# Performance work log

Measured on AMD Instinct MI355X. Metric: run time of the kernel, lower is better.

The kernel has to match this reference:

```python
import jax, jax.numpy as jnp
import numpy as np

N = 100000
E = 3200000
IN_C = 128
HID = 128


def setup_inputs() -> dict:
    key = jax.random.key(0)
    k1, k2, k3, k4, k5 = jax.random.split(key, 5)
    x = jax.random.normal(k1, (N, IN_C), dtype=jnp.float32)
    edge_index = jax.random.randint(k2, (2, E), 0, N, dtype=jnp.int64)
    edge_weight = jax.random.uniform(k3, (E,), dtype=jnp.float32)
    # GCNConv linear weight [out, in] (applied as x @ W.T), glorot-ish scale
    W = jax.random.normal(k4, (HID, IN_C), dtype=jnp.float32) / np.sqrt(IN_C)
    bias = jnp.zeros((HID,), dtype=jnp.float32)
    # PReLU per-channel alpha, torch default init 0.25
    alpha = jnp.full((HID,), 0.25, dtype=jnp.float32)
    return {"x": x, "edge_index": edge_index, "edge_weight": edge_weight,
            "W": W, "bias": bias, "alpha": alpha}


def reference(x, edge_index, edge_weight, W, bias, alpha):
    n = x.shape[0]
    # gcn_norm with self-loops (fill value 1.0)
    loop_idx = jnp.arange(n, dtype=edge_index.dtype)
    row = jnp.concatenate([edge_index[0], loop_idx])  # source
    col = jnp.concatenate([edge_index[1], loop_idx])  # target
    ew = jnp.concatenate([edge_weight, jnp.ones((n,), dtype=edge_weight.dtype)])
    deg = jax.ops.segment_sum(ew, col, num_segments=n)  # in-degree by weight
    dinv = jnp.where(deg > 0, jax.lax.rsqrt(deg), 0.0)
    norm = dinv[row] * ew * dinv[col]  # [E+N]
    # linear transform first (GCNConv order), then gather-scatter aggregation
    h = x @ W.T  # [N, HID]
    msgs = norm[:, None] * h[row]  # [E+N, HID]
    out = jax.ops.segment_sum(msgs, col, num_segments=n) + bias  # [N, HID]
    # PReLU with per-channel alpha
    return jnp.where(out > 0, out, alpha * out)
```

## Files before the change

### kernel.cpp

```cpp
#include <hip/hip_runtime.h>


#define NBLK    512
#define MAXBKT  1600
#define QSCALE  32767.0f
#define Q9      511.0f
#define SBS     16

typedef float vfloat2 __attribute__((ext_vector_type(2)));

__device__ __forceinline__ unsigned bf16pack2(float a, float b) {
    unsigned ua = __float_as_uint(a);
    ua = (ua + 0x7fffu + ((ua >> 16) & 1u)) >> 16;
    unsigned ub = __float_as_uint(b);
    ub = (ub + 0x7fffu + ((ub >> 16) & 1u)) >> 16;
    return ua | (ub << 16);
}

__device__ __forceinline__ float2 bf16unpack2(unsigned u) {
    return make_float2(__uint_as_float(u << 16),
                       __uint_as_float(u & 0xffff0000u));
}

__global__ __launch_bounds__(256) void p1_hist(const int* __restrict__ col,
                                               unsigned* __restrict__ hist,
                                               int e, int nbkt, int epb) {
    __shared__ unsigned lh[MAXBKT];
    int b = blockIdx.x;
    for (int k = threadIdx.x; k < nbkt; k += 256) lh[k] = 0;
    __syncthreads();
    int s = b * epb, en = s + epb; if (en > e) en = e;
    for (int i = s + threadIdx.x; i < en; i += 256)
        atomicAdd(&lh[col[i] >> 6], 1u);
    __syncthreads();
    for (int k = threadIdx.x; k < nbkt; k += 256)
        hist[(size_t)k * NBLK + b] = lh[k];
}

__global__ __launch_bounds__(1024) void scan_partial2(
    const unsigned* __restrict__ a, unsigned* __restrict__ part, int m) {
    __shared__ unsigned red[1024];
    int t = threadIdx.x, i = blockIdx.x * 1024 + t;
    red[t] = (i < m) ? a[i] : 0;
    __syncthreads();
    #pragma unroll
    for (int d = 512; d > 0; d >>= 1) {
        if (t < d) red[t] += red[t + d];
        __syncthreads();
    }
    if (t == 0) part[blockIdx.x] = red[0];
}

__global__ __launch_bounds__(1024) void scan_base2(
    unsigned* __restrict__ part, int nb, int* __restrict__ offs, int n, int e) {
    __shared__ unsigned s[1024];
    int t = threadIdx.x;
    unsigned v = (t < nb) ? part[t] : 0;
    s[t] = v;
    __syncthreads();
    for (int d = 1; d < 1024; d <<= 1) {
        unsigned add = (t >= d) ? s[t - d] : 0;
        __syncthreads();
        s[t] += add;
        __syncthreads();
    }
    if (t < nb) part[t] = s[t] - v;
    if (t == 0) offs[n] = e;
}

__global__ __launch_bounds__(1024) void scan_write2(
    unsigned* __restrict__ a, const unsigned* __restrict__ part, int m) {
    __shared__ unsigned s[1024];
    int t = threadIdx.x, i = blockIdx.x * 1024 + t;
    unsigned v = (i < m) ? a[i] : 0;
    s[t] = v;
    __syncthreads();
    for (int d = 1; d < 1024; d <<= 1) {
        unsigned add = (t >= d) ? s[t - d] : 0;
        __syncthreads();
        s[t] += add;
        __syncthreads();
    }
    if (i < m) a[i] = part[blockIdx.x] + s[t] - v;
}

__global__ __launch_bounds__(256) void fused_p2_gemm(
    const int* __restrict__ col, const int* __restrict__ row,
    const float* __restrict__ ew, const unsigned* __restrict__ base,
    unsigned* __restrict__ pay, int e, int nbkt, int epb,
    const float* __restrict__ x, const float* __restrict__ W,
    unsigned* __restrict__ h, int n) {
    __shared__ float smem[128 * 128];
    int bid = blockIdx.x;
    int t = threadIdx.x;

    if (bid < NBLK) {
        unsigned* lbase = (unsigned*)smem;
        unsigned* lcur  = (unsigned*)smem + MAXBKT;
        int b = bid;
        for (int k = t; k < nbkt; k += 256) {
            lbase[k] = base[(size_t)k * NBLK + b];
            lcur[k] = 0;
        }
        __syncthreads();
        int s = b * epb, en = s + epb; if (en > e) en = e;
        for (int i = s + t; i < en; i += 256) {
            int c = col[i];
            int bk = c >> 6;
            unsigned q = (unsigned)(ew[i] * Q9 + 0.5f);
            unsigned rk = atomicAdd(&lcur[bk], 1u);
            pay[(size_t)lbase[bk] + rk] =
                ((unsigned)(c & 63) << 26) | ((unsigned)row[i] << 9) | q;
        }
        return;
    }

    float (*Wt)[128] = (float (*)[128])smem;
    const float4* W4 = (const float4*)W;
    #pragma unroll
    for (int it = 0; it < 16; ++it) {
        int i = t + it * 256;
        float4 v = W4[i];
        int o  = i >> 5;
        int kb = (i & 31) << 2;
        Wt[kb + 0][o ^ (((kb + 0) & 7) << 2)] = v.x;
        Wt[kb + 1][o ^ (((kb + 1) & 7) << 2)] = v.y;
        Wt[kb + 2][o ^ (((kb + 2) & 7) << 2)] = v.z;
        Wt[kb + 3][o ^ (((kb + 3) & 7) << 2)] = v.w;
    }
    __syncthreads();

    int tc = t & 31;
    int rs = t >> 5;
    int r0 = (bid - NBLK) * 64 + rs * 8;
    if (r0 >= n) return;
    const float4* x4 = (const float4*)x;

    float acc[8][4];
    #pragma unroll
    for (int ri = 0; ri < 8; ++ri)
        #pragma unroll
        for (int j = 0; j < 4; ++j) acc[ri][j] = 0.0f;

    int rcnt = n - r0; if (rcnt > 8) rcnt = 8;

    if (rcnt == 8) {
        for (int kq = 0; kq < 32; ++kq) {
            int kb = kq << 2;
            float4 wv0 = *(const float4*)&Wt[kb + 0][(4 * tc) ^ (((kb + 0) & 7) << 2)];
            float4 wv1 = *(const float4*)&Wt[kb + 1][(4 * tc) ^ (((kb + 1) & 7) << 2)];
            float4 wv2 = *(const float4*)&Wt[kb + 2][(4 * tc) ^ (((kb + 2) & 7) << 2)];
            float4 wv3 = *(const float4*)&Wt[kb + 3][(4 * tc) ^ (((kb + 3) & 7) << 2)];
            #pragma unroll
            for (int ri = 0; ri < 8; ++ri) {
                float4 xv = x4[(size_t)(r0 + ri) * 32 + kq];
                acc[ri][0] += xv.x * wv0.x + xv.y * wv1.x + xv.z * wv2.x + xv.w * wv3.x;
                acc[ri][1] += xv.x * wv0.y + xv.y * wv1.y + xv.z * wv2.y + xv.w * wv3.y;
                acc[ri][2] += xv.x * wv0.z + xv.y * wv1.z + xv.z * wv2.z + xv.w * wv3.z;
                acc[ri][3] += xv.x * wv0.w + xv.y * wv1.w + xv.z * wv2.w + xv.w * wv3.w;
            }
        }
        uint2* h2 = (uint2*)h;
        #pragma unroll
        for (int ri = 0; ri < 8; ++ri)
            h2[(size_t)(r0 + ri) * 32 + tc] =
                make_uint2(bf16pack2(acc[ri][0], acc[ri][1]),
                           bf16pack2(acc[ri][2], acc[ri][3]));
    } else {
        for (int kq = 0; kq < 32; ++kq) {
            int kb = kq << 2;
            float4 wv0 = *(const float4*)&Wt[kb + 0][(4 * tc) ^ (((kb + 0) & 7) << 2)];
            float4 wv1 = *(const float4*)&Wt[kb + 1][(4 * tc) ^ (((kb + 1) & 7) << 2)];
            float4 wv2 = *(const float4*)&Wt[kb + 2][(4 * tc) ^ (((kb + 2) & 7) << 2)];
            float4 wv3 = *(const float4*)&Wt[kb + 3][(4 * tc) ^ (((kb + 3) & 7) << 2)];
            for (int ri = 0; ri < rcnt; ++ri) {
                float4 xv = x4[(size_t)(r0 + ri) * 32 + kq];
                acc[ri][0] += xv.x * wv0.x + xv.y * wv1.x + xv.z * wv2.x + xv.w * wv3.x;
                acc[ri][1] += xv.x * wv0.y + xv.y * wv1.y + xv.z * wv2.y + xv.w * wv3.y;
                acc[ri][2] += xv.x * wv0.z + xv.y * wv1.z + xv.z * wv2.z + xv.w * wv3.z;
                acc[ri][3] += xv.x * wv0.w + xv.y * wv1.w + xv.z * wv2.w + xv.w * wv3.w;
            }
        }
        uint2* h2 = (uint2*)h;
        for (int ri = 0; ri < rcnt; ++ri)
            h2[(size_t)(r0 + ri) * 32 + tc] =
                make_uint2(bf16pack2(acc[ri][0], acc[ri][1]),
                           bf16pack2(acc[ri][2], acc[ri][3]));
    }
}

__global__ __launch_bounds__(256) void p3_build(
    const unsigned* __restrict__ pay,
    const unsigned* __restrict__ histBase,
    unsigned* __restrict__ csr, int* __restrict__ offs,
    float* __restrict__ dinv, int n, int nbkt, int e) {
    __shared__ unsigned cnt[64][SBS], lofs[64][SBS], cur[64][SBS];
    __shared__ unsigned wsum[64], tbase[64], ttot[64];
    int bk = blockIdx.x;
    int zs = (int)histBase[(size_t)bk * NBLK];
    int ze = (bk + 1 < nbkt) ? (int)histBase[(size_t)(bk + 1) * NBLK] : e;
    int t = threadIdx.x;
    for (int k = t; k < 64 * SBS; k += 256) {
        (&cnt[0][0])[k] = 0;
        (&cur[0][0])[k] = 0;
    }
    if (t < 64) wsum[t] = 0;
    __syncthreads();
    for (int p = zs + t; p < ze; p += 256) {
        unsigned v = pay[p];
        int l = (int)(v >> 26);
        int sb = (int)(((v >> 9) & 0x1ffffu) >> 13);
        atomicAdd(&cnt[l][sb], 1u);
        atomicAdd(&wsum[l], v & 0x1ffu);
    }
    __syncthreads();
    if (t < 64) {
        unsigned s = 0;
        #pragma unroll
        for (int j = 0; j < SBS; ++j) s += cnt[t][j];
        ttot[t] = s;
    }
    __syncthreads();
    if (t == 0) {
        unsigned run = 0;
        for (int l = 0; l < 64; ++l) { tbase[l] = run; run += ttot[l]; }
    }
    __syncthreads();
    if (t < 64) {
        unsigned run = tbase[t];
        #pragma unroll
        for (int j = 0; j < SBS; ++j) { lofs[t][j] = run; run += cnt[t][j]; }
    }
    __syncthreads();
    for (int p = zs + t; p < ze; p += 256) {
        unsigned v = pay[p];
        int l = (int)(v >> 26);
        unsigned lo = v & 0x03ffffffu;
        int sb = (int)((lo >> 9) >> 13);
        unsigned rk = atomicAdd(&cur[l][sb], 1u);
        csr[zs + lofs[l][sb] + rk] = lo;
    }
    if (t < 64) {
        int node = bk * 64 + t;
        if (node < n) {
            offs[node] = zs + (int)tbase[t];
            float dg = 1.0f + (float)wsum[t] * (1.0f / Q9);
            dinv[node] = rsqrtf(dg);
        }
    }
}

__global__ __launch_bounds__(256) void csr2_fill(const unsigned* __restrict__ csr,
                                                 const float* __restrict__ dinv,
                                                 unsigned* __restrict__ csr2, int e) {
    int i = blockIdx.x * 256 + threadIdx.x;
    if (i < e) {
        unsigned v = csr[i];
        unsigned src = v >> 9;
        float a = dinv[src] * ((float)(v & 0x1ffu) * (1.0f / Q9));
        csr2[i] = (src << 15) | (unsigned)(a * QSCALE + 0.5f);
    }
}

__global__ __launch_bounds__(256) void aggregate_kernel(
    const unsigned* __restrict__ h, const unsigned* __restrict__ csr2,
    const int* __restrict__ offs, const float* __restrict__ dinv,
    const float* __restrict__ bias, const float* __restrict__ alpha,
    float* __restrict__ out, int n, int swzq) {
    int bid = blockIdx.x;
    int sb  = swzq ? ((bid & 7) * swzq + (bid >> 3)) : bid;
    int w = sb * 4 + (threadIdx.x >> 6);
    if (w >= n) return;
    int lane = threadIdx.x & 63;

    int beg = __builtin_amdgcn_readfirstlane(offs[w]);
    int end = __builtin_amdgcn_readfirstlane(offs[w + 1]);
    float ax = 0.0f, ay = 0.0f;

    int i = beg;
    int end4 = beg + ((end - beg) & ~3);
    for (; i < end4; i += 4) {
        unsigned v0 = __builtin_nontemporal_load(&csr2[i]);
        unsigned v1 = __builtin_nontemporal_load(&csr2[i + 1]);
        unsigned v2 = __builtin_nontemporal_load(&csr2[i + 2]);
        unsigned v3 = __builtin_nontemporal_load(&csr2[i + 3]);
        unsigned u0 = h[(size_t)(v0 >> 15) * 64 + lane];
        unsigned u1 = h[(size_t)(v1 >> 15) * 64 + lane];
        unsigned u2 = h[(size_t)(v2 >> 15) * 64 + lane];
        unsigned u3 = h[(size_t)(v3 >> 15) * 64 + lane];
        float a0 = (float)(v0 & 0x7fffu) * (1.0f / QSCALE);
        float a1 = (float)(v1 & 0x7fffu) * (1.0f / QSCALE);
        float a2 = (float)(v2 & 0x7fffu) * (1.0f / QSCALE);
        float a3 = (float)(v3 & 0x7fffu) * (1.0f / QSCALE);
        float2 h0 = bf16unpack2(u0), h1 = bf16unpack2(u1);
        float2 h2 = bf16unpack2(u2), h3 = bf16unpack2(u3);
        ax += a0 * h0.x; ay += a0 * h0.y;
        ax += a1 * h1.x; ay += a1 * h1.y;
        ax += a2 * h2.x; ay += a2 * h2.y;
        ax += a3 * h3.x; ay += a3 * h3.y;
    }
    for (; i < end; ++i) {
        unsigned v = __builtin_nontemporal_load(&csr2[i]);
        unsigned u = h[(size_t)(v >> 15) * 64 + lane];
        float a = (float)(v & 0x7fffu) * (1.0f / QSCALE);
        float2 hv = bf16unpack2(u);
        ax += a * hv.x; ay += a * hv.y;
    }

    float dc = dinv[w];
    float2 hc = bf16unpack2(h[(size_t)w * 64 + lane]);
    ax += dc * hc.x; ay += dc * hc.y;

    float2 bv = ((const float2*)bias)[lane];
    float2 av = ((const float2*)alpha)[lane];
    float ox = ax * dc + bv.x;
    float oy = ay * dc + bv.y;
    ox = ox > 0.0f ? ox : av.x * ox;
    oy = oy > 0.0f ? oy : av.y * oy;
    vfloat2 ov; ov.x = ox; ov.y = oy;
    __builtin_nontemporal_store(ov,
        (vfloat2*)&((float2*)out)[(size_t)w * 64 + lane]);
}

extern "C" void kernel_launch(void* const* d_in, const int* in_sizes, int n_in,
                              void* d_out, int out_size, void* d_ws, size_t ws_size,
                              hipStream_t stream) {
    const float* x     = (const float*)d_in[0];
    const int*   ei    = (const int*)d_in[1];
    const float* ew    = (const float*)d_in[2];
    const float* W     = (const float*)d_in[3];
    const float* bias  = (const float*)d_in[4];
    const float* alpha = (const float*)d_in[5];
    float* out = (float*)d_out;

    const int n = in_sizes[0] / 128;
    const int e = in_sizes[1] / 2;
    const int* row = ei;
    const int* col = ei + e;

    const int nbkt = (n + 63) >> 6;
    const int m    = nbkt * NBLK;
    const int epb  = (e + NBLK - 1) / NBLK;
    const int nb2  = (m + 1023) / 1024;

    char* ws = (char*)d_ws;
    size_t off = 0;
    auto alloc = [&](size_t bytes) -> char* {
        char* p = ws + off;
        off = (off + bytes + 255) & ~(size_t)255;
        return p;
    };
    unsigned* hist = (unsigned*)alloc((size_t)m * 4);
    unsigned* part = (unsigned*)alloc((size_t)1024 * 4);
    int*      offs = (int*)     alloc((size_t)(n + 1) * 4);
    float*    dinv = (float*)   alloc((size_t)n * 4);
    unsigned* pay  = (unsigned*)alloc((size_t)e * 4);
    unsigned* csr  = (unsigned*)alloc((size_t)e * 4);
    unsigned* csr2 = (unsigned*)alloc((size_t)e * 4);
    unsigned* h    = (unsigned*)alloc((size_t)n * 128 * 2);
    (void)ws_size; (void)n_in; (void)out_size;

    int gg = (n + 63) / 64;

    p1_hist<<<NBLK, 256, 0, stream>>>(col, hist, e, nbkt, epb);
    scan_partial2<<<nb2, 1024, 0, stream>>>(hist, part, m);
    scan_base2<<<1, 1024, 0, stream>>>(part, nb2, offs, n, e);
    scan_write2<<<nb2, 1024, 0, stream>>>(hist, part, m);
    fused_p2_gemm<<<NBLK + gg, 256, 0, stream>>>(col, row, ew, hist, pay,
                                                 e, nbkt, epb, x, W, h, n);
    p3_build<<<nbkt, 256, 0, stream>>>(pay, hist, csr, offs, dinv, n, nbkt, e);
    csr2_fill<<<(e + 255) / 256, 256, 0, stream>>>(csr, dinv, csr2, e);

    int ga = (n + 3) / 4;
    int swzq = (ga % 8 == 0) ? ga / 8 : 0;
    aggregate_kernel<<<ga, 256, 0, stream>>>(h, csr2, offs, dinv,
                                             bias, alpha, out, n, swzq);
}
```

Measured before the change: 288.1 us.

## Split fused scatter/GEMM kernel, shrink partition blocks, add nontemporal edge loads

Splits the fused scatter+GEMM kernel into a standalone 1024-thread scatter kernel and a GEMM kernel launched after the CSR build. It also cuts the partition block count from 512 to 128 with 1024 threads each, and marks streaming edge reads as nontemporal. Fewer, larger blocks shrink the histogram and scan arrays, and the scatter kernel no longer carries the GEMM's 64KB shared-memory footprint. In exchange, the GEMM no longer overlaps with the scatter, and each block's local atomics see more contention.

Result: slower. 332.4 us (+15.4%).

```diff
diff --git a/kernel.cpp b/kernel.cpp
--- a/kernel.cpp
+++ b/kernel.cpp
@@ -1,7 +1,7 @@
 #include <hip/hip_runtime.h>
 
 
-#define NBLK    512
+#define NBLK    128
 #define MAXBKT  1600
 #define QSCALE  32767.0f
 #define Q9      511.0f
@@ -22,18 +22,19 @@
                        __uint_as_float(u & 0xffff0000u));
 }
 
-__global__ __launch_bounds__(256) void p1_hist(const int* __restrict__ col,
-                                               unsigned* __restrict__ hist,
-                                               int e, int nbkt, int epb) {
+__global__ __launch_bounds__(1024) void p1_hist(const int* __restrict__ col,
+                                                unsigned* __restrict__ hist,
+                                                int e, int nbkt, int epb) {
     __shared__ unsigned lh[MAXBKT];
     int b = blockIdx.x;
-    for (int k = threadIdx.x; k < nbkt; k += 256) lh[k] = 0;
+    int t = threadIdx.x;
+    for (int k = t; k < nbkt; k += 1024) lh[k] = 0;
     __syncthreads();
     int s = b * epb, en = s + epb; if (en > e) en = e;
-    for (int i = s + threadIdx.x; i < en; i += 256)
-        atomicAdd(&lh[col[i] >> 6], 1u);
-    __syncthreads();
-    for (int k = threadIdx.x; k < nbkt; k += 256)
+    for (int i = s + t; i < en; i += 1024)
+        atomicAdd(&lh[__builtin_nontemporal_load(&col[i]) >> 6], 1u);
+    __syncthreads();
+    for (int k = t; k < nbkt; k += 1024)
         hist[(size_t)k * NBLK + b] = lh[k];
 }
 
@@ -84,38 +85,110 @@
     if (i < m) a[i] = part[blockIdx.x] + s[t] - v;
 }
 
-__global__ __launch_bounds__(256) void fused_p2_gemm(
+__global__ __launch_bounds__(1024) void p2_scatter(
     const int* __restrict__ col, const int* __restrict__ row,
     const float* __restrict__ ew, const unsigned* __restrict__ base,
-    unsigned* __restrict__ pay, int e, int nbkt, int epb,
-    const float* __restrict__ x, const float* __restrict__ W,
-    unsigned* __restrict__ h, int n) {
-    __shared__ float smem[128 * 128];
-    int bid = blockIdx.x;
-    int t = threadIdx.x;
-
-    if (bid < NBLK) {
-        unsigned* lbase = (unsigned*)smem;
-        unsigned* lcur  = (unsigned*)smem + MAXBKT;
-        int b = bid;
-        for (int k = t; k < nbkt; k += 256) {
-            lbase[k] = base[(size_t)k * NBLK + b];
-            lcur[k] = 0;
+    unsigned* __restrict__ pay, int e, int nbkt, int epb) {
+    __shared__ unsigned lbase[MAXBKT];
+    __shared__ unsigned lcur[MAXBKT];
+    int b = blockIdx.x;
+    int t = threadIdx.x;
+    for (int k = t; k < nbkt; k += 1024) {
+        lbase[k] = base[(size_t)k * NBLK + b];
+        lcur[k] = 0;
+    }
+    __syncthreads();
+    int s = b * epb, en = s + epb; if (en > e) en = e;
+    for (int i = s + t; i < en; i += 1024) {
+        int c = __builtin_nontemporal_load(&col[i]);
+        int r = __builtin_nontemporal_load(&row[i]);
+        float w = __builtin_nontemporal_load(&ew[i]);
+        int bk = c >> 6;
+        unsigned q = (unsigned)(w * Q9 + 0.5f);
+        unsigned rk = atomicAdd(&lcur[bk], 1u);
+        pay[(size_t)lbase[bk] + rk] =
+            ((unsigned)(c & 63) << 26) | ((unsigned)r << 9) | q;
+    }
+}
+
+__global__ __launch_bounds__(256) void p3_build(
+    const unsigned* __restrict__ pay,
+    const unsigned* __restrict__ histBase,
+    unsigned* __restrict__ csr, int* __restrict__ offs,
+    float* __restrict__ dinv, int n, int nbkt, int e) {
+    __shared__ unsigned cnt[64][SBS], lofs[64][SBS], cur[64][SBS];
+    __shared__ unsigned wsum[64], tbase[64], ttot[64];
+    int bk = blockIdx.x;
+    int zs = (int)histBase[(size_t)bk * NBLK];
+    int ze = (bk + 1 < nbkt) ? (int)histBase[(size_t)(bk + 1) * NBLK] : e;
+    int t = threadIdx.x;
+    for (int k = t; k < 64 * SBS; k += 256) {
+        (&cnt[0][0])[k] = 0;
+        (&cur[0][0])[k] = 0;
+    }
+    if (t < 64) wsum[t] = 0;
+    __syncthreads();
+    for (int p = zs + t; p < ze; p += 256) {
+        unsigned v = pay[p];
+        int l = (int)(v >> 26);
+        int sb = (int)(((v >> 9) & 0x1ffffu) >> 13);
+        atomicAdd(&cnt[l][sb], 1u);
+        atomicAdd(&wsum[l], v & 0x1ffu);
+    }
+    __syncthreads();
+    if (t < 64) {
+        unsigned s = 0;
+        #pragma unroll
+        for (int j = 0; j < SBS; ++j) s += cnt[t][j];
+        ttot[t] = s;
+    }
+    __syncthreads();
+    if (t == 0) {
+        unsigned run = 0;
+        for (int l = 0; l < 64; ++l) { tbase[l] = run; run += ttot[l]; }
+    }
+    __syncthreads();
+    if (t < 64) {
+        unsigned run = tbase[t];
+        #pragma unroll
+        for (int j = 0; j < SBS; ++j) { lofs[t][j] = run; run += cnt[t][j]; }
+    }
+    __syncthreads();
+    for (int p = zs + t; p < ze; p += 256) {
+        unsigned v = pay[p];
+        int l = (int)(v >> 26);
+        unsigned lo = v & 0x03ffffffu;
+        int sb = (int)((lo >> 9) >> 13);
+        unsigned rk = atomicAdd(&cur[l][sb], 1u);
+        csr[zs + lofs[l][sb] + rk] = lo;
+    }
+    if (t < 64) {
+        int node = bk * 64 + t;
+        if (node < n) {
+            offs[node] = zs + (int)tbase[t];
+            float dg = 1.0f + (float)wsum[t] * (1.0f / Q9);
+            dinv[node] = rsqrtf(dg);
         }
-        __syncthreads();
-        int s = b * epb, en = s + epb; if (en > e) en = e;
-        for (int i = s + t; i < en; i += 256) {
-            int c = col[i];
-            int bk = c >> 6;
-            unsigned q = (unsigned)(ew[i] * Q9 + 0.5f);
-            unsigned rk = atomicAdd(&lcur[bk], 1u);
-            pay[(size_t)lbase[bk] + rk] =
-                ((unsigned)(c & 63) << 26) | ((unsigned)row[i] << 9) | q;
-        }
-        return;
-    }
-
-    float (*Wt)[128] = (float (*)[128])smem;
+    }
+}
+
+__global__ __launch_bounds__(256) void csr2_fill(const unsigned* __restrict__ csr,
+                                                 const float* __restrict__ dinv,
+                                                 unsigned* __restrict__ csr2, int e) {
+    int i = blockIdx.x * 256 + threadIdx.x;
+    if (i < e) {
+        unsigned v = __builtin_nontemporal_load(&csr[i]);
+        unsigned src = v >> 9;
+        float a = dinv[src] * ((float)(v & 0x1ffu) * (1.0f / Q9));
+        csr2[i] = (src << 15) | (unsigned)(a * QSCALE + 0.5f);
+    }
+}
+
+__global__ __launch_bounds__(256) void gemm_kernel(const float* __restrict__ x,
+                                                   const float* __restrict__ W,
+                                                   unsigned* __restrict__ h, int n) {
+    __shared__ float Wt[128][128];
+    int t = threadIdx.x;
     const float4* W4 = (const float4*)W;
     #pragma unroll
     for (int it = 0; it < 16; ++it) {
@@ -132,7 +205,7 @@
 
     int tc = t & 31;
     int rs = t >> 5;
-    int r0 = (bid - NBLK) * 64 + rs * 8;
+    int r0 = blockIdx.x * 64 + rs * 8;
     if (r0 >= n) return;
     const float4* x4 = (const float4*)x;
 
@@ -189,79 +262,6 @@
     }
 }
 
-__global__ __launch_bounds__(256) void p3_build(
-    const unsigned* __restrict__ pay,
-    const unsigned* __restrict__ histBase,
-    unsigned* __restrict__ csr, int* __restrict__ offs,
-    float* __restrict__ dinv, int n, int nbkt, int e) {
-    __shared__ unsigned cnt[64][SBS], lofs[64][SBS], cur[64][SBS];
-    __shared__ unsigned wsum[64], tbase[64], ttot[64];
-    int bk = blockIdx.x;
-    int zs = (int)histBase[(size_t)bk * NBLK];
-    int ze = (bk + 1 < nbkt) ? (int)histBase[(size_t)(bk + 1) * NBLK] : e;
-    int t = threadIdx.x;
-    for (int k = t; k < 64 * SBS; k += 256) {
-        (&cnt[0][0])[k] = 0;
-        (&cur[0][0])[k] = 0;
-    }
-    if (t < 64) wsum[t] = 0;
-    __syncthreads();
-    for (int p = zs + t; p < ze; p += 256) {
-        unsigned v = pay[p];
-        int l = (int)(v >> 26);
-        int sb = (int)(((v >> 9) & 0x1ffffu) >> 13);
-        atomicAdd(&cnt[l][sb], 1u);
-        atomicAdd(&wsum[l], v & 0x1ffu);
-    }
-    __syncthreads();
-    if (t < 64) {
-        unsigned s = 0;
-        #pragma unroll
-        for (int j = 0; j < SBS; ++j) s += cnt[t][j];
-        ttot[t] = s;
-    }
-    __syncthreads();
-    if (t == 0) {
-        unsigned run = 0;
-        for (int l = 0; l < 64; ++l) { tbase[l] = run; run += ttot[l]; }
-    }
-    __syncthreads();
-    if (t < 64) {
-        unsigned run = tbase[t];
-        #pragma unroll
-        for (int j = 0; j < SBS; ++j) { lofs[t][j] = run; run += cnt[t][j]; }
-    }
-    __syncthreads();
-    for (int p = zs + t; p < ze; p += 256) {
-        unsigned v = pay[p];
-        int l = (int)(v >> 26);
-        unsigned lo = v & 0x03ffffffu;
-        int sb = (int)((lo >> 9) >> 13);
-        unsigned rk = atomicAdd(&cur[l][sb], 1u);
-        csr[zs + lofs[l][sb] + rk] = lo;
-    }
-    if (t < 64) {
-        int node = bk * 64 + t;
-        if (node < n) {
-            offs[node] = zs + (int)tbase[t];
-            float dg = 1.0f + (float)wsum[t] * (1.0f / Q9);
-            dinv[node] = rsqrtf(dg);
-        }
-    }
-}
-
-__global__ __launch_bounds__(256) void csr2_fill(const unsigned* __restrict__ csr,
-                                                 const float* __restrict__ dinv,
-                                                 unsigned* __restrict__ csr2, int e) {
-    int i = blockIdx.x * 256 + threadIdx.x;
-    if (i < e) {
-        unsigned v = csr[i];
-        unsigned src = v >> 9;
-        float a = dinv[src] * ((float)(v & 0x1ffu) * (1.0f / Q9));
-        csr2[i] = (src << 15) | (unsigned)(a * QSCALE + 0.5f);
-    }
-}
-
 __global__ __launch_bounds__(256) void aggregate_kernel(
     const unsigned* __restrict__ h, const unsigned* __restrict__ csr2,
     const int* __restrict__ offs, const float* __restrict__ dinv,
@@ -360,16 +360,16 @@
     unsigned* h    = (unsigned*)alloc((size_t)n * 128 * 2);
     (void)ws_size; (void)n_in; (void)out_size;
 
-    int gg = (n + 63) / 64;
-
-    p1_hist<<<NBLK, 256, 0, stream>>>(col, hist, e, nbkt, epb);
+    p1_hist<<<NBLK, 1024, 0, stream>>>(col, hist, e, nbkt, epb);
     scan_partial2<<<nb2, 1024, 0, stream>>>(hist, part, m);
     scan_base2<<<1, 1024, 0, stream>>>(part, nb2, offs, n, e);
     scan_write2<<<nb2, 1024, 0, stream>>>(hist, part, m);
-    fused_p2_gemm<<<NBLK + gg, 256, 0, stream>>>(col, row, ew, hist, pay,
-                                                 e, nbkt, epb, x, W, h, n);
+    p2_scatter<<<NBLK, 1024, 0, stream>>>(col, row, ew, hist, pay, e, nbkt, epb);
     p3_build<<<nbkt, 256, 0, stream>>>(pay, hist, csr, offs, dinv, n, nbkt, e);
     csr2_fill<<<(e + 255) / 256, 256, 0, stream>>>(csr, dinv, csr2, e);
+
+    int gg = (n + 63) / 64;
+    gemm_kernel<<<gg, 256, 0, stream>>>(x, W, h, n);
 
     int ga = (n + 3) / 4;
     int swzq = (ga % 8 == 0) ? ga / 8 : 0;
```
